# Performance work log

Measured on AMD Instinct MI355X. Metric: run time of the kernel, lower is better.

## Reference

```python
import jax, jax.numpy as jnp
import numpy as np

N_NODES = 50000
N_EDGES = 800000
IN_DIM = 128
HID = 32
HEADS = 4
EMB = 64
NEG_SLOPE = 0.2
LN_EPS = 1e-5


def setup_inputs() -> dict:
    key = jax.random.key(0)
    ks = jax.random.split(key, 16)
    s = 0.1
    inp = {
        'x': jax.random.normal(ks[0], (N_NODES, IN_DIM), dtype=jnp.float32),
        'edge_index': jax.random.randint(ks[1], (2, N_EDGES), 0, N_NODES, dtype=jnp.int64),
        # GATConv 1: in=128 -> heads=4, out_per_head=32, concat -> 128
        'W1': jax.random.normal(ks[2], (IN_DIM, HEADS * HID), dtype=jnp.float32) * s,
        'att_src1': jax.random.normal(ks[3], (HEADS, HID), dtype=jnp.float32) * s,
        'att_dst1': jax.random.normal(ks[4], (HEADS, HID), dtype=jnp.float32) * s,
        'b1': jnp.zeros((HEADS * HID,), dtype=jnp.float32),
        'gamma1': jnp.ones((HEADS * HID,), dtype=jnp.float32),
        'beta1': jnp.zeros((HEADS * HID,), dtype=jnp.float32),
        # GATConv 2: in=128 -> heads=1, out=64, concat=False
        'W2': jax.random.normal(ks[5], (HEADS * HID, EMB), dtype=jnp.float32) * s,
        'att_src2': jax.random.normal(ks[6], (1, EMB), dtype=jnp.float32) * s,
        'att_dst2': jax.random.normal(ks[7], (1, EMB), dtype=jnp.float32) * s,
        'b2': jnp.zeros((EMB,), dtype=jnp.float32),
        'gamma2': jnp.ones((EMB,), dtype=jnp.float32),
        'beta2': jnp.zeros((EMB,), dtype=jnp.float32),
    }
    return inp


def _gat_conv(x, src, dst, W, att_src, att_dst):
    # x: [N, F_in]; src/dst: [E'] (self loops included); W: [F_in, H*C]
    N = x.shape[0]
    H, C = att_src.shape
    h = (x @ W).reshape(N, H, C)                          # [N, H, C]
    a_s = jnp.sum(h * att_src, axis=-1)                   # [N, H]
    a_d = jnp.sum(h * att_dst, axis=-1)                   # [N, H]
    e = jax.nn.leaky_relu(a_s[src] + a_d[dst], NEG_SLOPE) # [E', H]
    # segment softmax over destination-node neighborhoods
    m = jax.ops.segment_max(e, dst, num_segments=N)       # [N, H]
    ex = jnp.exp(e - m[dst])
    den = jax.ops.segment_sum(ex, dst, num_segments=N)    # [N, H]
    alpha = ex / den[dst]                                  # [E', H]
    msg = h[src] * alpha[:, :, None]                       # [E', H, C]
    return jax.ops.segment_sum(msg, dst, num_segments=N)  # [N, H, C]


def _layer_norm(x, gamma, beta):
    mu = jnp.mean(x, axis=-1, keepdims=True)
    var = jnp.var(x, axis=-1, keepdims=True)
    return (x - mu) * jax.lax.rsqrt(var + LN_EPS) * gamma + beta


def reference(x, edge_index, W1, att_src1, att_dst1, b1, gamma1, beta1,
              W2, att_src2, att_dst2, b2, gamma2, beta2):
    N = x.shape[0]
    loops = jnp.arange(N, dtype=edge_index.dtype)
    src = jnp.concatenate([edge_index[0], loops])  # PyG add_self_loops=True
    dst = jnp.concatenate([edge_index[1], loops])

    # gat1: heads=4, concat=True
    h1 = _gat_conv(x, src, dst, W1, att_src1, att_dst1)   # [N, 4, 32]
    h1 = h1.reshape(N, -1) + b1                            # [N, 128]
    h1 = jax.nn.relu(_layer_norm(h1, gamma1, beta1))
    # dropout is identity in eval mode

    # gat2: heads=1, concat=False (mean over the single head)
    h2 = _gat_conv(h1, src, dst, W2, att_src2, att_dst2)  # [N, 1, 64]
    h2 = h2.mean(axis=1) + b2                              # [N, 64]
    return _layer_norm(h2, gamma2, beta2)
```

## Files before the change

### kernel.cpp

```cpp
#include <hip/hip_runtime.h>
#include <hip/hip_bf16.h>
#include <hip/hip_fp16.h>
#include <math.h>

#define N_NODES 50000
#define N_EDGES 800000
#define HEADS 4
#define HID 32
#define D1 128
#define D2 64
#define NEG_SLOPE 0.2f
#define LN_EPS 1e-5f

#define GB1N 782
#define GB2N 782

#define NCHUNK 128
#define CHE (N_EDGES / NCHUNK)
#define HWORDS (N_NODES / 2)
#define HVEC (HWORDS / 4)
#define CAPS 64
#define CSCANB ((HWORDS + 255) / 256)

typedef __attribute__((ext_vector_type(8))) short bf16x8;
typedef __attribute__((ext_vector_type(4))) float f32x4;

__device__ __forceinline__ float lrelu(float x) { return x > 0.f ? x : NEG_SLOPE * x; }

__device__ __forceinline__ short f2bf_s(float x) {
    union { __hip_bfloat16 h; short s; } u;
    u.h = __float2bfloat16(x);
    return u.s;
}
__device__ __forceinline__ float bfs2f(short s) {
    union { unsigned u; float f; } v;
    v.u = ((unsigned)(unsigned short)s) << 16;
    return v.f;
}
__device__ __forceinline__ void split_bf(float x, short& hi, short& lo) {
    hi = f2bf_s(x);
    lo = f2bf_s(x - bfs2f(hi));
}
__device__ __forceinline__ void acc8h(float* acc, uint4 r, float w) {
    union { uint4 u; __half2 h[4]; } q;
    q.u = r;
#pragma unroll
    for (int i = 0; i < 4; ++i) {
        acc[2 * i]     = fmaf(__low2float(q.h[i]), w, acc[2 * i]);
        acc[2 * i + 1] = fmaf(__high2float(q.h[i]), w, acc[2 * i + 1]);
    }
}
__device__ __forceinline__ void acc4h(float* acc, uint2 r, float w) {
    union { uint2 u; __half2 h[2]; } q;
    q.u = r;
    acc[0] = fmaf(__low2float(q.h[0]), w, acc[0]);
    acc[1] = fmaf(__high2float(q.h[0]), w, acc[1]);
    acc[2] = fmaf(__low2float(q.h[1]), w, acc[2]);
    acc[3] = fmaf(__high2float(q.h[1]), w, acc[3]);
}

__global__ __launch_bounds__(512) void hist_kernel(const int* __restrict__ dst,
                                                   unsigned* __restrict__ hist) {
    __shared__ unsigned cnt[HWORDS];
    int c = blockIdx.x;
    for (int i = threadIdx.x; i < HVEC; i += 512) ((uint4*)cnt)[i] = make_uint4(0, 0, 0, 0);
    __syncthreads();
    int base = c * CHE;
    for (int t = threadIdx.x; t < CHE; t += 512) {
        int d = dst[base + t];
        atomicAdd(&cnt[d >> 1], 1u << ((d & 1) * 16));
    }
    __syncthreads();
    uint4* out = (uint4*)(hist + (size_t)c * HWORDS);
    for (int i = threadIdx.x; i < HVEC; i += 512) out[i] = ((const uint4*)cnt)[i];
}

__global__ __launch_bounds__(256, 3) void gemm1_mfma_cscan_kernel(
    const float* __restrict__ X, const float* __restrict__ W,
    __half* __restrict__ Y,
    const float* __restrict__ att_src, const float* __restrict__ att_dst,
    float* __restrict__ a_s, float* __restrict__ a_d,
    unsigned* __restrict__ hist, unsigned* __restrict__ degp) {
    if (blockIdx.x >= GB1N) {
        int wword = (blockIdx.x - GB1N) * 256 + threadIdx.x;
        if (wword >= HWORDS) return;
        unsigned run = 0;
#pragma unroll 8
        for (int c = 0; c < NCHUNK; ++c) {
            unsigned v = hist[(size_t)c * HWORDS + wword];
            hist[(size_t)c * HWORDS + wword] = run;
            run += v;
        }
        degp[wword] = run;
        return;
    }
    int tid = threadIdx.x;
    int w = tid >> 6;
    int l = tid & 63;
    int lr = l & 15;
    int lq = l >> 4;

    bf16x8 bh[2][4], bl[2][4];
#pragma unroll
    for (int nt = 0; nt < 2; ++nt)
#pragma unroll
        for (int kt = 0; kt < 4; ++kt) {
            int colIdx = (2 * w + nt) * 16 + lr;
            int rowBase = kt * 32 + lq * 8;
#pragma unroll
            for (int s = 0; s < 8; ++s) {
                short hi, lo;
                split_bf(W[(rowBase + s) * 128 + colIdx], hi, lo);
                bh[nt][kt][s] = hi;
                bl[nt][kt][s] = lo;
            }
        }

    int r0 = blockIdx.x * 64;
    float asv0 = att_src[w * 32 + lr], asv1 = att_src[w * 32 + 16 + lr];
    float adv0 = att_dst[w * 32 + lr], adv1 = att_dst[w * 32 + 16 + lr];

#pragma unroll
    for (int mt = 0; mt < 4; ++mt) {
        int rb = r0 + mt * 16;
        int row = rb + lr;
        if (row >= N_NODES) row = N_NODES - 1;
        const float* xr = X + (size_t)row * 128;
        f32x4 acc0 = {0.f, 0.f, 0.f, 0.f};
        f32x4 acc1 = {0.f, 0.f, 0.f, 0.f};
#pragma unroll
        for (int kt = 0; kt < 4; ++kt) {
            int cb = kt * 32 + lq * 8;
            float4 f0 = *(const float4*)(xr + cb);
            float4 f1 = *(const float4*)(xr + cb + 4);
            float xs[8] = {f0.x, f0.y, f0.z, f0.w, f1.x, f1.y, f1.z, f1.w};
            bf16x8 ah, al;
#pragma unroll
            for (int s = 0; s < 8; ++s) {
                short h_, l_;
                split_bf(xs[s], h_, l_);
                ah[s] = h_;
                al[s] = l_;
            }
            acc0 = __builtin_amdgcn_mfma_f32_16x16x32_bf16(ah, bh[0][kt], acc0, 0, 0, 0);
            acc1 = __builtin_amdgcn_mfma_f32_16x16x32_bf16(ah, bh[1][kt], acc1, 0, 0, 0);
            acc0 = __builtin_amdgcn_mfma_f32_16x16x32_bf16(al, bh[0][kt], acc0, 0, 0, 0);
            acc1 = __builtin_amdgcn_mfma_f32_16x16x32_bf16(al, bh[1][kt], acc1, 0, 0, 0);
            acc0 = __builtin_amdgcn_mfma_f32_16x16x32_bf16(ah, bl[0][kt], acc0, 0, 0, 0);
            acc1 = __builtin_amdgcn_mfma_f32_16x16x32_bf16(ah, bl[1][kt], acc1, 0, 0, 0);
        }
#pragma unroll
        for (int reg = 0; reg < 4; ++reg) {
            int r = rb + lq * 4 + reg;
            float v0 = acc0[reg], v1 = acc1[reg];
            float ps = v0 * asv0 + v1 * asv1;
            float pd = v0 * adv0 + v1 * adv1;
#pragma unroll
            for (int m = 1; m < 16; m <<= 1) {
                ps += __shfl_xor(ps, m, 64);
                pd += __shfl_xor(pd, m, 64);
            }
            if (r < N_NODES) {
                Y[(size_t)r * 128 + w * 32 + lr] = __float2half(v0);
                Y[(size_t)r * 128 + w * 32 + 16 + lr] = __float2half(v1);
                if (lr == 0) {
                    a_s[r * 4 + w] = ps;
                    a_d[r * 4 + w] = pd;
                }
            }
        }
    }
}

__global__ __launch_bounds__(512) void scatter_sorted_kernel(const int* __restrict__ src,
                                                             const int* __restrict__ dst,
                                                             const unsigned* __restrict__ hist,
                                                             int* __restrict__ col) {
    __shared__ unsigned cnt[HWORDS];
    int c = blockIdx.x;
    const uint4* row = (const uint4*)(hist + (size_t)c * HWORDS);
    for (int i = threadIdx.x; i < HVEC; i += 512) ((uint4*)cnt)[i] = row[i];
    __syncthreads();
    int base = c * CHE;
    for (int t = threadIdx.x; t < CHE; t += 512) {
        int d = dst[base + t];
        unsigned old = atomicAdd(&cnt[d >> 1], 1u << ((d & 1) * 16));
        unsigned pos = (old >> ((d & 1) * 16)) & 0xffffu;
        if (pos < CAPS) col[d * CAPS + pos] = src[base + t];
    }
}

__global__ __launch_bounds__(256, 3) void gemm2_mfma_kernel(
    const __half* __restrict__ X, const float* __restrict__ W,
    __half* __restrict__ Y,
    const float* __restrict__ att_src, const float* __restrict__ att_dst,
    float* __restrict__ a_s, float* __restrict__ a_d) {
    __shared__ float psh[4][64];
    __shared__ float pdh[4][64];
    int tid = threadIdx.x;
    int w = tid >> 6;
    int l = tid & 63;
    int lr = l & 15;
    int lq = l >> 4;

    bf16x8 bh[4], bl[4];
#pragma unroll
    for (int kt = 0; kt < 4; ++kt) {
        int colIdx = w * 16 + lr;
        int rowBase = kt * 32 + lq * 8;
#pragma unroll
        for (int s = 0; s < 8; ++s) {
            short hi, lo;
            split_bf(W[(rowBase + s) * 64 + colIdx], hi, lo);
            bh[kt][s] = hi;
            bl[kt][s] = lo;
        }
    }

    int r0 = blockIdx.x * 64;
    float asv = att_src[w * 16 + lr];
    float adv = att_dst[w * 16 + lr];

    f32x4 acc[4];
#pragma unroll
    for (int mt = 0; mt < 4; ++mt) acc[mt] = (f32x4){0.f, 0.f, 0.f, 0.f};

#pragma unroll
    for (int mt = 0; mt < 4; ++mt) {
        int row = r0 + mt * 16 + lr;
        if (row >= N_NODES) row = N_NODES - 1;
        const __half* xr = X + (size_t)row * 128;
#pragma unroll
        for (int kt = 0; kt < 4; ++kt) {
            int cb = kt * 32 + lq * 8;
            union { uint4 u; __half2 h[4]; } q;
            q.u = *(const uint4*)(xr + cb);
            float xs[8];
#pragma unroll
            for (int i = 0; i < 4; ++i) {
                xs[2 * i] = __low2float(q.h[i]);
                xs[2 * i + 1] = __high2float(q.h[i]);
            }
            bf16x8 ah, al;
#pragma unroll
            for (int s = 0; s < 8; ++s) {
                short h_, l_;
                split_bf(xs[s], h_, l_);
                ah[s] = h_;
                al[s] = l_;
            }
            acc[mt] = __builtin_amdgcn_mfma_f32_16x16x32_bf16(ah, bh[kt], acc[mt], 0, 0, 0);
            acc[mt] = __builtin_amdgcn_mfma_f32_16x16x32_bf16(al, bh[kt], acc[mt], 0, 0, 0);
            acc[mt] = __builtin_amdgcn_mfma_f32_16x16x32_bf16(ah, bl[kt], acc[mt], 0, 0, 0);
        }
    }

#pragma unroll
    for (int mt = 0; mt < 4; ++mt) {
#pragma unroll
        for (int reg = 0; reg < 4; ++reg) {
            int r = r0 + mt * 16 + lq * 4 + reg;
            float v = acc[mt][reg];
            float ps = v * asv;
            float pd = v * adv;
#pragma unroll
            for (int m = 1; m < 16; m <<= 1) {
                ps += __shfl_xor(ps, m, 64);
                pd += __shfl_xor(pd, m, 64);
            }
            if (r < N_NODES) Y[(size_t)r * 64 + w * 16 + lr] = __float2half(v);
            if (lr == 0) {
                psh[w][mt * 16 + lq * 4 + reg] = ps;
                pdh[w][mt * 16 + lq * 4 + reg] = pd;
            }
        }
    }
    __syncthreads();
    if (tid < 64) {
        int r = r0 + tid;
        if (r < N_NODES) {
            a_s[r] = psh[0][tid] + psh[1][tid] + psh[2][tid] + psh[3][tid];
            a_d[r] = pdh[0][tid] + pdh[1][tid] + pdh[2][tid] + pdh[3][tid];
        }
    }
}

__global__ __launch_bounds__(256) void agg1_kernel(const __half* __restrict__ h,
                                                   const float* __restrict__ a_s,
                                                   const float* __restrict__ a_d,
                                                   const unsigned* __restrict__ degp,
                                                   const int* __restrict__ col,
                                                   const float* __restrict__ b1,
                                                   const float* __restrict__ gamma,
                                                   const float* __restrict__ beta,
                                                   __half* __restrict__ out) {
    __shared__ int colsh[4][CAPS];
    __shared__ float wsh[4][CAPS * 4];
    int wv = threadIdx.x >> 6;
    int lane = threadIdx.x & 63;
    int n = blockIdx.x * 4 + wv;
    int nn = (n < N_NODES) ? n : N_NODES - 1;
    int eslot = lane >> 4;
    int ch = lane & 15;
    int head = ch >> 2;

    int deg = (int)((degp[nn >> 1] >> ((nn & 1) * 16)) & 0xffffu);
    if (deg > CAPS) deg = CAPS;
    int beg = nn * CAPS;
    const float4 ad4 = *(const float4*)&a_d[nn * 4];
    uint4 rself = *(const uint4*)(h + (size_t)nn * 128 + ch * 8);

    int s_pre = (lane < deg) ? col[beg + lane] : nn;
    int sp0 = __shfl(s_pre, eslot, 64);
    int sp1 = __shfl(s_pre, eslot + 4, 64);
    uint4 rp0 = *(const uint4*)(h + (size_t)sp0 * 128 + ch * 8);
    uint4 rp1 = *(const uint4*)(h + (size_t)sp1 * 128 + ch * 8);

    float den0 = 0.f, den1 = 0.f, den2 = 0.f, den3 = 0.f;
    {
        const float4 as4 = *(const float4*)&a_s[s_pre * 4];
        float w0 = __expf(lrelu(as4.x + ad4.x));
        float w1 = __expf(lrelu(as4.y + ad4.y));
        float w2 = __expf(lrelu(as4.z + ad4.z));
        float w3 = __expf(lrelu(as4.w + ad4.w));
        if (lane < deg) {
            colsh[wv][lane] = s_pre;
            *(float4*)&wsh[wv][lane * 4] = make_float4(w0, w1, w2, w3);
            den0 = w0; den1 = w1; den2 = w2; den3 = w3;
        }
    }
    float adh = (head == 0) ? ad4.x : (head == 1) ? ad4.y : (head == 2) ? ad4.z : ad4.w;
    float wself = __expf(lrelu(a_s[nn * 4 + head] + adh));

    float acc[8];
#pragma unroll
    for (int i = 0; i < 8; ++i) acc[i] = 0.f;
    if (eslot < deg)     acc8h(acc, rp0, wsh[wv][eslot * 4 + head]);
    if (eslot + 4 < deg) acc8h(acc, rp1, wsh[wv][(eslot + 4) * 4 + head]);
    int t = eslot + 8;
    for (; t + 4 < deg; t += 8) {
        int sa = colsh[wv][t], sb = colsh[wv][t + 4];
        float wa = wsh[wv][t * 4 + head], wb = wsh[wv][(t + 4) * 4 + head];
        uint4 ra = *(const uint4*)(h + (size_t)sa * 128 + ch * 8);
        uint4 rb = *(const uint4*)(h + (size_t)sb * 128 + ch * 8);
        acc8h(acc, ra, wa);
        acc8h(acc, rb, wb);
    }
    if (t < deg) {
        int sa = colsh[wv][t];
        float wa = wsh[wv][t * 4 + head];
        uint4 ra = *(const uint4*)(h + (size_t)sa * 128 + ch * 8);
        acc8h(acc, ra, wa);
    }
    if (eslot == 0) acc8h(acc, rself, wself);

#pragma unroll
    for (int i = 0; i < 8; ++i) {
        acc[i] += __shfl_xor(acc[i], 16, 64);
        acc[i] += __shfl_xor(acc[i], 32, 64);
    }
#pragma unroll
    for (int m = 1; m < 64; m <<= 1) {
        den0 += __shfl_xor(den0, m, 64);
        den1 += __shfl_xor(den1, m, 64);
        den2 += __shfl_xor(den2, m, 64);
        den3 += __shfl_xor(den3, m, 64);
    }
    float den_h = ((head == 0) ? den0 : (head == 1) ? den1 : (head == 2) ? den2 : den3) + wself;

    float inv = 1.f / den_h;
    const float4 b1a = *(const float4*)&b1[ch * 8];
    const float4 b1b = *(const float4*)&b1[ch * 8 + 4];
    float v[8];
    v[0] = acc[0] * inv + b1a.x; v[1] = acc[1] * inv + b1a.y;
    v[2] = acc[2] * inv + b1a.z; v[3] = acc[3] * inv + b1a.w;
    v[4] = acc[4] * inv + b1b.x; v[5] = acc[5] * inv + b1b.y;
    v[6] = acc[6] * inv + b1b.z; v[7] = acc[7] * inv + b1b.w;

    float s1 = 0.f, s2 = 0.f;
#pragma unroll
    for (int i = 0; i < 8; ++i) { s1 += v[i]; s2 += v[i] * v[i]; }
#pragma unroll
    for (int m = 1; m < 64; m <<= 1) {
        s1 += __shfl_xor(s1, m, 64);
        s2 += __shfl_xor(s2, m, 64);
    }
    float mean = s1 * (1.f / 512.f);
    float var = s2 * (1.f / 512.f) - mean * mean;
    float r = rsqrtf(var + LN_EPS);
    int c0 = ch * 8 + eslot * 2;
    const float2 g2 = *(const float2*)&gamma[c0];
    const float2 be2 = *(const float2*)&beta[c0];
    float ox = fmaxf(0.f, (v[eslot * 2] - mean) * r * g2.x + be2.x);
    float oy = fmaxf(0.f, (v[eslot * 2 + 1] - mean) * r * g2.y + be2.y);
    if (n < N_NODES) {
        __half2 p;
        p.x = __float2half(ox);
        p.y = __float2half(oy);
        *(__half2*)&out[(size_t)n * 128 + c0] = p;
    }
}

__global__ __launch_bounds__(256) void agg2_kernel(const __half* __restrict__ h,
                                                   const float* __restrict__ a_s,
                                                   const float* __restrict__ a_d,
                                                   const unsigned* __restrict__ degp,
                                                   const int* __restrict__ col,
                                                   const float* __restrict__ b2,
                                                   const float* __restrict__ gamma,
                                                   const float* __restrict__ beta,
                                                   float* __restrict__ out) {
    __shared__ int colsh[4][CAPS];
    __shared__ float wsh[4][CAPS];
    int wv = threadIdx.x >> 6;
    int lane = threadIdx.x & 63;
    int n = blockIdx.x * 4 + wv;
    int nn = (n < N_NODES) ? n : N_NODES - 1;
    int eslot = lane >> 4;
    int q = lane & 15;

    int deg = (int)((degp[nn >> 1] >> ((nn & 1) * 16)) & 0xffffu);
    if (deg > CAPS) deg = CAPS;
    int beg = nn * CAPS;
    float adh = a_d[nn];
    uint2 rself = *(const uint2*)(h + (size_t)nn * 64 + q * 4);

    float den = 0.f;
    if (lane < deg) {
        int s = col[beg + lane];
        float w = __expf(lrelu(a_s[s] + adh));
        colsh[wv][lane] = s;
        wsh[wv][lane] = w;
        den = w;
    }
#pragma unroll
    for (int m = 1; m < 64; m <<= 1) den += __shfl_xor(den, m, 64);
    float wself = __expf(lrelu(a_s[nn] + adh));
    den += wself;

    float acc[4];
#pragma unroll
    for (int i = 0; i < 4; ++i) acc[i] = 0.f;
    int t = eslot;
    for (; t + 12 < deg; t += 16) {
        int s0 = colsh[wv][t], s1 = colsh[wv][t + 4], s2 = colsh[wv][t + 8], s3 = colsh[wv][t + 12];
        float w0 = wsh[wv][t], w1 = wsh[wv][t + 4], w2 = wsh[wv][t + 8], w3 = wsh[wv][t + 12];
        uint2 r0 = *(const uint2*)(h + (size_t)s0 * 64 + q * 4);
        uint2 r1 = *(const uint2*)(h + (size_t)s1 * 64 + q * 4);
        uint2 r2 = *(const uint2*)(h + (size_t)s2 * 64 + q * 4);
        uint2 r3 = *(const uint2*)(h + (size_t)s3 * 64 + q * 4);
        acc4h(acc, r0, w0);
        acc4h(acc, r1, w1);
        acc4h(acc, r2, w2);
        acc4h(acc, r3, w3);
    }
    for (; t + 4 < deg; t += 8) {
        int s0 = colsh[wv][t], s1 = colsh[wv][t + 4];
        float w0 = wsh[wv][t], w1 = wsh[wv][t + 4];
        uint2 r0 = *(const uint2*)(h + (size_t)s0 * 64 + q * 4);
        uint2 r1 = *(const uint2*)(h + (size_t)s1 * 64 + q * 4);
        acc4h(acc, r0, w0);
        acc4h(acc, r1, w1);
    }
    if (t < deg) {
        int s0 = colsh[wv][t];
        float w0 = wsh[wv][t];
        uint2 r0 = *(const uint2*)(h + (size_t)s0 * 64 + q * 4);
        acc4h(acc, r0, w0);
    }
    if (eslot == 0) acc4h(acc, rself, wself);

#pragma unroll
    for (int i = 0; i < 4; ++i) {
        acc[i] += __shfl_xor(acc[i], 16, 64);
        acc[i] += __shfl_xor(acc[i], 32, 64);
    }
    float inv = 1.f / den;
    const float4 b2v = *(const float4*)&b2[q * 4];
    float v[4];
    v[0] = acc[0] * inv + b2v.x;
    v[1] = acc[1] * inv + b2v.y;
    v[2] = acc[2] * inv + b2v.z;
    v[3] = acc[3] * inv + b2v.w;

    float s1 = 0.f, s2 = 0.f;
#pragma unroll
    for (int i = 0; i < 4; ++i) { s1 += v[i]; s2 += v[i] * v[i]; }
#pragma unroll
    for (int m = 1; m < 64; m <<= 1) {
        s1 += __shfl_xor(s1, m, 64);
        s2 += __shfl_xor(s2, m, 64);
    }
    float mean = s1 * (1.f / 256.f);
    float var = s2 * (1.f / 256.f) - mean * mean;
    float r = rsqrtf(var + LN_EPS);
    if (n < N_NODES && eslot == 0) {
        const float4 g4 = *(const float4*)&gamma[q * 4];
        const float4 be4 = *(const float4*)&beta[q * 4];
        float4 o;
        o.x = (v[0] - mean) * r * g4.x + be4.x;
        o.y = (v[1] - mean) * r * g4.y + be4.y;
        o.z = (v[2] - mean) * r * g4.z + be4.z;
        o.w = (v[3] - mean) * r * g4.w + be4.w;
        *(float4*)&out[(size_t)n * 64 + q * 4] = o;
    }
}

extern "C" void kernel_launch(void* const* d_in, const int* in_sizes, int n_in,
                              void* d_out, int out_size, void* d_ws, size_t ws_size,
                              hipStream_t stream) {
    const float* x        = (const float*)d_in[0];
    const int*   ei       = (const int*)d_in[1];
    const float* W1       = (const float*)d_in[2];
    const float* att_src1 = (const float*)d_in[3];
    const float* att_dst1 = (const float*)d_in[4];
    const float* b1       = (const float*)d_in[5];
    const float* gamma1   = (const float*)d_in[6];
    const float* beta1    = (const float*)d_in[7];
    const float* W2       = (const float*)d_in[8];
    const float* att_src2 = (const float*)d_in[9];
    const float* att_dst2 = (const float*)d_in[10];
    const float* b2       = (const float*)d_in[11];
    const float* gamma2   = (const float*)d_in[12];
    const float* beta2    = (const float*)d_in[13];
    const int* src = ei;
    const int* dst = ei + N_EDGES;
    float* out = (float*)d_out;

    char* ws = (char*)d_ws;
    size_t off = 0;
    auto alloc = [&](size_t bytes) -> void* {
        void* p = ws + off;
        off += bytes;
        off = (off + 255) & ~(size_t)255;
        return p;
    };
    __half* h1pre = (__half*)alloc((size_t)N_NODES * 128 * 2);
    __half* h2pre = (__half*)alloc((size_t)N_NODES * 64 * 2);
    float* a_s1   = (float*)alloc((size_t)N_NODES * 4 * 4);
    float* a_d1   = (float*)alloc((size_t)N_NODES * 4 * 4);
    __half* h1n   = (__half*)alloc((size_t)N_NODES * 128 * 2);
    float* a_s2   = (float*)alloc((size_t)N_NODES * 4);
    float* a_d2   = (float*)alloc((size_t)N_NODES * 4);
    unsigned* hist = (unsigned*)alloc((size_t)NCHUNK * HWORDS * 4);
    unsigned* degp = (unsigned*)alloc((size_t)HWORDS * 4);
    int* col      = (int*)alloc((size_t)N_NODES * CAPS * 4);

    const int NWB = (N_NODES + 3) / 4;

    hist_kernel<<<NCHUNK, 512, 0, stream>>>(dst, hist);
    gemm1_mfma_cscan_kernel<<<GB1N + CSCANB, 256, 0, stream>>>(
        x, W1, h1pre, att_src1, att_dst1, a_s1, a_d1, hist, degp);
    scatter_sorted_kernel<<<NCHUNK, 512, 0, stream>>>(src, dst, hist, col);

    agg1_kernel<<<NWB, 256, 0, stream>>>(h1pre, a_s1, a_d1, degp, col, b1, gamma1, beta1, h1n);

    gemm2_mfma_kernel<<<GB2N, 256, 0, stream>>>(
        h1n, W2, h2pre, att_src2, att_dst2, a_s2, a_d2);
    agg2_kernel<<<NWB, 256, 0, stream>>>(h2pre, a_s2, a_d2, degp, col, b2, gamma2, beta2, out);
}
```

Baseline: 233.0 us.

## Fuse layer-1 aggregation with layer-2 GEMM in a single kernel

Merges agg1 and gemm2 into one kernel. Each block normalizes its 4 node rows into shared memory, then runs a small fp16 MFMA against W2 to produce h2pre and the layer-2 attention scores. This removes the h1n intermediate round trip through global memory and one kernel launch. In exchange, every block reloads W2 (8K floats) from cache, 12 of the 16 MFMA rows are zero padding, and an added block-wide sync can stall the aggregation waves. It also switches from the 3-pass split-bf16 scheme to a single fp16 MFMA, which lowers accuracy.

```diff
diff --git a/kernel.cpp b/kernel.cpp
--- a/kernel.cpp
+++ b/kernel.cpp
@@ -13,7 +13,6 @@
 #define LN_EPS 1e-5f
 
 #define GB1N 782
-#define GB2N 782
 
 #define NCHUNK 128
 #define CHE (N_EDGES / NCHUNK)
@@ -23,6 +22,7 @@
 #define CSCANB ((HWORDS + 255) / 256)
 
 typedef __attribute__((ext_vector_type(8))) short bf16x8;
+typedef __attribute__((ext_vector_type(8))) _Float16 f16x8;
 typedef __attribute__((ext_vector_type(4))) float f32x4;
 
 __device__ __forceinline__ float lrelu(float x) { return x > 0.f ? x : NEG_SLOPE * x; }
@@ -190,112 +190,24 @@
     }
 }
 
-__global__ __launch_bounds__(256, 3) void gemm2_mfma_kernel(
-    const __half* __restrict__ X, const float* __restrict__ W,
-    __half* __restrict__ Y,
-    const float* __restrict__ att_src, const float* __restrict__ att_dst,
-    float* __restrict__ a_s, float* __restrict__ a_d) {
-    __shared__ float psh[4][64];
-    __shared__ float pdh[4][64];
-    int tid = threadIdx.x;
-    int w = tid >> 6;
-    int l = tid & 63;
-    int lr = l & 15;
-    int lq = l >> 4;
-
-    bf16x8 bh[4], bl[4];
-#pragma unroll
-    for (int kt = 0; kt < 4; ++kt) {
-        int colIdx = w * 16 + lr;
-        int rowBase = kt * 32 + lq * 8;
-#pragma unroll
-        for (int s = 0; s < 8; ++s) {
-            short hi, lo;
-            split_bf(W[(rowBase + s) * 64 + colIdx], hi, lo);
-            bh[kt][s] = hi;
-            bl[kt][s] = lo;
-        }
-    }
-
-    int r0 = blockIdx.x * 64;
-    float asv = att_src[w * 16 + lr];
-    float adv = att_dst[w * 16 + lr];
-
-    f32x4 acc[4];
-#pragma unroll
-    for (int mt = 0; mt < 4; ++mt) acc[mt] = (f32x4){0.f, 0.f, 0.f, 0.f};
-
-#pragma unroll
-    for (int mt = 0; mt < 4; ++mt) {
-        int row = r0 + mt * 16 + lr;
-        if (row >= N_NODES) row = N_NODES - 1;
-        const __half* xr = X + (size_t)row * 128;
-#pragma unroll
-        for (int kt = 0; kt < 4; ++kt) {
-            int cb = kt * 32 + lq * 8;
-            union { uint4 u; __half2 h[4]; } q;
-            q.u = *(const uint4*)(xr + cb);
-            float xs[8];
-#pragma unroll
-            for (int i = 0; i < 4; ++i) {
-                xs[2 * i] = __low2float(q.h[i]);
-                xs[2 * i + 1] = __high2float(q.h[i]);
-            }
-            bf16x8 ah, al;
-#pragma unroll
-            for (int s = 0; s < 8; ++s) {
-                short h_, l_;
-                split_bf(xs[s], h_, l_);
-                ah[s] = h_;
-                al[s] = l_;
-            }
-            acc[mt] = __builtin_amdgcn_mfma_f32_16x16x32_bf16(ah, bh[kt], acc[mt], 0, 0, 0);
-            acc[mt] = __builtin_amdgcn_mfma_f32_16x16x32_bf16(al, bh[kt], acc[mt], 0, 0, 0);
-            acc[mt] = __builtin_amdgcn_mfma_f32_16x16x32_bf16(ah, bl[kt], acc[mt], 0, 0, 0);
-        }
-    }
-
-#pragma unroll
-    for (int mt = 0; mt < 4; ++mt) {
-#pragma unroll
-        for (int reg = 0; reg < 4; ++reg) {
-            int r = r0 + mt * 16 + lq * 4 + reg;
-            float v = acc[mt][reg];
-            float ps = v * asv;
-            float pd = v * adv;
-#pragma unroll
-            for (int m = 1; m < 16; m <<= 1) {
-                ps += __shfl_xor(ps, m, 64);
-                pd += __shfl_xor(pd, m, 64);
-            }
-            if (r < N_NODES) Y[(size_t)r * 64 + w * 16 + lr] = __float2half(v);
-            if (lr == 0) {
-                psh[w][mt * 16 + lq * 4 + reg] = ps;
-                pdh[w][mt * 16 + lq * 4 + reg] = pd;
-            }
-        }
-    }
-    __syncthreads();
-    if (tid < 64) {
-        int r = r0 + tid;
-        if (r < N_NODES) {
-            a_s[r] = psh[0][tid] + psh[1][tid] + psh[2][tid] + psh[3][tid];
-            a_d[r] = pdh[0][tid] + pdh[1][tid] + pdh[2][tid] + pdh[3][tid];
-        }
-    }
-}
-
-__global__ __launch_bounds__(256) void agg1_kernel(const __half* __restrict__ h,
-                                                   const float* __restrict__ a_s,
-                                                   const float* __restrict__ a_d,
-                                                   const unsigned* __restrict__ degp,
-                                                   const int* __restrict__ col,
-                                                   const float* __restrict__ b1,
-                                                   const float* __restrict__ gamma,
-                                                   const float* __restrict__ beta,
-                                                   __half* __restrict__ out) {
+__global__ __launch_bounds__(256) void agg1_gemm2_kernel(const __half* __restrict__ h,
+                                                         const float* __restrict__ a_s,
+                                                         const float* __restrict__ a_d,
+                                                         const unsigned* __restrict__ degp,
+                                                         const int* __restrict__ col,
+                                                         const float* __restrict__ b1,
+                                                         const float* __restrict__ gamma,
+                                                         const float* __restrict__ beta,
+                                                         const float* __restrict__ W2,
+                                                         const float* __restrict__ att_src2,
+                                                         const float* __restrict__ att_dst2,
+                                                         __half* __restrict__ h2pre,
+                                                         float* __restrict__ a_s2,
+                                                         float* __restrict__ a_d2) {
     __shared__ int colsh[4][CAPS];
     __shared__ float wsh[4][CAPS * 4];
+    __shared__ _Float16 rowS[4][128];
+    __shared__ float psh2[4][4], pdh2[4][4];
     int wv = threadIdx.x >> 6;
     int lane = threadIdx.x & 63;
     int n = blockIdx.x * 4 + wv;
@@ -387,17 +299,71 @@
     }
     float mean = s1 * (1.f / 512.f);
     float var = s2 * (1.f / 512.f) - mean * mean;
-    float r = rsqrtf(var + LN_EPS);
-    int c0 = ch * 8 + eslot * 2;
-    const float2 g2 = *(const float2*)&gamma[c0];
-    const float2 be2 = *(const float2*)&beta[c0];
-    float ox = fmaxf(0.f, (v[eslot * 2] - mean) * r * g2.x + be2.x);
-    float oy = fmaxf(0.f, (v[eslot * 2 + 1] - mean) * r * g2.y + be2.y);
-    if (n < N_NODES) {
-        __half2 p;
-        p.x = __float2half(ox);
-        p.y = __float2half(oy);
-        *(__half2*)&out[(size_t)n * 128 + c0] = p;
+    float rstd = rsqrtf(var + LN_EPS);
+
+    if (eslot == 0) {
+        const float4 g1a = *(const float4*)&gamma[ch * 8];
+        const float4 g1b = *(const float4*)&gamma[ch * 8 + 4];
+        const float4 be1a = *(const float4*)&beta[ch * 8];
+        const float4 be1b = *(const float4*)&beta[ch * 8 + 4];
+        float gg[8] = {g1a.x, g1a.y, g1a.z, g1a.w, g1b.x, g1b.y, g1b.z, g1b.w};
+        float bb[8] = {be1a.x, be1a.y, be1a.z, be1a.w, be1b.x, be1b.y, be1b.z, be1b.w};
+#pragma unroll
+        for (int i = 0; i < 8; ++i) {
+            float o = fmaxf(0.f, (v[i] - mean) * rstd * gg[i] + bb[i]);
+            rowS[wv][ch * 8 + i] = (_Float16)o;
+        }
+    }
+    __syncthreads();
+
+    f16x8 bfr[4];
+#pragma unroll
+    for (int kt = 0; kt < 4; ++kt) {
+        int rowBase = kt * 32 + eslot * 8;
+#pragma unroll
+        for (int s = 0; s < 8; ++s)
+            bfr[kt][s] = (_Float16)W2[(rowBase + s) * 64 + wv * 16 + ch];
+    }
+    f32x4 acc2 = {0.f, 0.f, 0.f, 0.f};
+#pragma unroll
+    for (int kt = 0; kt < 4; ++kt) {
+        f16x8 a;
+        if (ch < 4) {
+            a = *(const f16x8*)&rowS[ch][kt * 32 + eslot * 8];
+        } else {
+#pragma unroll
+            for (int s = 0; s < 8; ++s) a[s] = (_Float16)0.f;
+        }
+        acc2 = __builtin_amdgcn_mfma_f32_16x16x32_f16(a, bfr[kt], acc2, 0, 0, 0);
+    }
+
+    float as2v = att_src2[wv * 16 + ch];
+    float ad2v = att_dst2[wv * 16 + ch];
+#pragma unroll
+    for (int reg = 0; reg < 4; ++reg) {
+        float hv = acc2[reg];
+        float ps = (eslot == 0) ? hv * as2v : 0.f;
+        float pd = (eslot == 0) ? hv * ad2v : 0.f;
+#pragma unroll
+        for (int m = 1; m < 16; m <<= 1) {
+            ps += __shfl_xor(ps, m, 64);
+            pd += __shfl_xor(pd, m, 64);
+        }
+        int node = blockIdx.x * 4 + reg;
+        if (eslot == 0 && node < N_NODES) {
+            h2pre[(size_t)node * 64 + wv * 16 + ch] = __float2half(hv);
+            if (ch == 0) { psh2[wv][reg] = ps; pdh2[wv][reg] = pd; }
+        }
+    }
+    __syncthreads();
+    if (threadIdx.x < 4) {
+        int node = blockIdx.x * 4 + (int)threadIdx.x;
+        if (node < N_NODES) {
+            a_s2[node] = psh2[0][threadIdx.x] + psh2[1][threadIdx.x] +
+                         psh2[2][threadIdx.x] + psh2[3][threadIdx.x];
+            a_d2[node] = pdh2[0][threadIdx.x] + pdh2[1][threadIdx.x] +
+                         pdh2[2][threadIdx.x] + pdh2[3][threadIdx.x];
+        }
     }
 }
 
@@ -539,7 +505,6 @@
     __half* h2pre = (__half*)alloc((size_t)N_NODES * 64 * 2);
     float* a_s1   = (float*)alloc((size_t)N_NODES * 4 * 4);
     float* a_d1   = (float*)alloc((size_t)N_NODES * 4 * 4);
-    __half* h1n   = (__half*)alloc((size_t)N_NODES * 128 * 2);
     float* a_s2   = (float*)alloc((size_t)N_NODES * 4);
     float* a_d2   = (float*)alloc((size_t)N_NODES * 4);
     unsigned* hist = (unsigned*)alloc((size_t)NCHUNK * HWORDS * 4);
@@ -553,9 +518,9 @@
         x, W1, h1pre, att_src1, att_dst1, a_s1, a_d1, hist, degp);
     scatter_sorted_kernel<<<NCHUNK, 512, 0, stream>>>(src, dst, hist, col);
 
-    agg1_kernel<<<NWB, 256, 0, stream>>>(h1pre, a_s1, a_d1, degp, col, b1, gamma1, beta1, h1n);
-
-    gemm2_mfma_kernel<<<GB2N, 256, 0, stream>>>(
-        h1n, W2, h2pre, att_src2, att_dst2, a_s2, a_d2);
+    agg1_gemm2_kernel<<<NWB, 256, 0, stream>>>(
+        h1pre, a_s1, a_d1, degp, col, b1, gamma1, beta1,
+        W2, att_src2, att_dst2, h2pre, a_s2, a_d2);
+
     agg2_kernel<<<NWB, 256, 0, stream>>>(h2pre, a_s2, a_d2, degp, col, b2, gamma2, beta2, out);
 }
```

Measured after the change: 236.8 us. Within noise of the previous version (+1.6%).
